# Kernel optimization log

Measured on AMD Instinct MI355X. Metric: run time of the kernel, lower is better.

The kernel has to match this reference:

```python
import jax, jax.numpy as jnp
import numpy as np

RADIUS, HEAD, SLOT, DIM = 16.0, 8, 112, 512

def _l2norm(x, axis):
    n = jnp.linalg.norm(x, axis=axis, keepdims=True)
    return x / jnp.maximum(n, 1e-12)

def _layernorm(x, g, b, eps=1e-5):
    mu = jnp.mean(x, axis=-1, keepdims=True)
    var = jnp.mean((x - mu) ** 2, axis=-1, keepdims=True)
    return (x - mu) / jnp.sqrt(var + eps) * g + b

def setup_inputs() -> dict:
    key = jax.random.key(0)
    ks = jax.random.split(key, 12)
    B, S = 32, 512
    return {
        "query": jax.random.normal(ks[0], (B, S, DIM), jnp.float32),
        "value": jax.random.normal(ks[1], (B, S, DIM), jnp.float32),
        "key_mem": jax.random.normal(ks[2], (HEAD * SLOT, DIM // HEAD), jnp.float32) * 0.5,
        "value_mem": jax.random.normal(ks[3], (SLOT, DIM), jnp.float32) * 0.5,
        "Wq": jax.random.normal(ks[4], (DIM, DIM), jnp.float32) * 0.02,
        "bq": jnp.zeros((DIM,), jnp.float32),
        "Wv": jax.random.normal(ks[5], (DIM, DIM), jnp.float32) * 0.02,
        "bv": jnp.zeros((DIM,), jnp.float32),
        "Wl": jax.random.normal(ks[6], (DIM, DIM * HEAD), jnp.float32) * 0.02,
        "bl": jnp.zeros((DIM,), jnp.float32),
        "g1": jnp.ones((DIM,), jnp.float32), "b1": jnp.zeros((DIM,), jnp.float32),
        "g2": jnp.ones((DIM,), jnp.float32), "b2": jnp.zeros((DIM,), jnp.float32),
        "g3": jnp.ones((DIM,), jnp.float32), "b3": jnp.zeros((DIM,), jnp.float32),
    }

def reference(query, value, key_mem, value_mem, Wq, bq, Wv, bv, Wl, bl,
              g1, b1, g2, b2, g3, b3):
    B, S, C = query.shape
    mq = query.reshape(B * S, C)                                   # (BS, 512)
    # --- key addressing (read path) ---
    key_norm = _l2norm(key_mem.reshape(HEAD, SLOT, -1), axis=2)    # (h, s, 64)
    eq = _l2norm((mq @ Wq.T + bq).reshape(B * S, HEAD, -1), axis=2)
    key_sim = jnp.einsum('bhd,hsd->bhs', eq, key_norm)             # (BS, h, s)
    key_add = jax.nn.softmax(RADIUS * key_sim, axis=2)
    m_head = jnp.einsum('bhs,sd->bhd', key_add,
                        jax.lax.stop_gradient(value_mem))          # (BS, h, 512)
    vir = _layernorm(m_head.reshape(B * S, HEAD * DIM) @ Wl.T + bl, g2, b2)
    te_fusion = _layernorm(query + vir.reshape(B, S, DIM), g1, b1)  # dropout = eval identity
    # --- value addressing (write/train path) ---
    mv = value.reshape(B * S, DIM)
    ev = jax.lax.stop_gradient(mv) @ Wv.T + bv
    value_norm = _l2norm(value_mem, axis=1)                        # (s, 512)
    value_sim = _l2norm(ev, axis=1) @ value_norm.T                 # (BS, s)
    value_add = jax.nn.softmax(RADIUS * value_sim, axis=1)
    aud = value_add @ value_mem                                    # (BS, 512)
    contrastive = 0.5 * jnp.abs(jnp.eye(SLOT, dtype=value_norm.dtype)
                                - value_norm @ value_norm.T).sum()[None]
    mvd = jax.lax.stop_gradient(mv)
    cos = (aud * mvd).sum(1) / jnp.maximum(
        jnp.linalg.norm(aud, axis=1) * jnp.linalg.norm(mvd, axis=1), 1e-8)
    recon = jnp.abs(1.0 - cos).reshape(B, S).sum(1)                # (B,)
    aud = _layernorm(aud, g3, b3)
    tr_fusion = _layernorm(query + aud.reshape(B, S, DIM), g1, b1)
    return (te_fusion, tr_fusion, recon, contrastive)
```

## Files before the change

### kernel.cpp

```cpp
#include <hip/hip_runtime.h>
#include <math.h>

#define DIMC   512
#define HEADS  8
#define SLOTS  112
#define HD     64
#define NROWS  16384
#define RADIUSF 16.0f

typedef short short8 __attribute__((ext_vector_type(8)));
typedef unsigned short ushort8 __attribute__((ext_vector_type(8)));
typedef float f32x4  __attribute__((ext_vector_type(4)));

__device__ __forceinline__ unsigned short f2bf(float f)
{
    unsigned u = __float_as_uint(f);
    unsigned r = (u + 0x7FFFu + ((u >> 16) & 1u)) >> 16;
    return (unsigned short)r;
}
__device__ __forceinline__ float bf2f(unsigned short h)
{
    return __uint_as_float((unsigned)h << 16);
}

#define DPP_ADD(x, ctrl, rmask)                                               \
    (x) += __int_as_float(__builtin_amdgcn_update_dpp(                        \
               0, __float_as_int(x), (ctrl), (rmask), 0xf, true))
#define DPP_MAX(x, ctrl, rmask)                                               \
    (x) = fmaxf((x), __int_as_float(__builtin_amdgcn_update_dpp(              \
               __float_as_int(x), __float_as_int(x), (ctrl), (rmask), 0xf,    \
               false)))

__device__ __forceinline__ float wsum64(float x)
{
    DPP_ADD(x, 0x111, 0xf);
    DPP_ADD(x, 0x112, 0xf);
    DPP_ADD(x, 0x114, 0xf);
    DPP_ADD(x, 0x118, 0xf);
    DPP_ADD(x, 0x142, 0xa);
    DPP_ADD(x, 0x143, 0xc);
    return __int_as_float(__builtin_amdgcn_readlane(__float_as_int(x), 63));
}

__device__ __forceinline__ float wmax64(float x)
{
    DPP_MAX(x, 0x111, 0xf);
    DPP_MAX(x, 0x112, 0xf);
    DPP_MAX(x, 0x114, 0xf);
    DPP_MAX(x, 0x118, 0xf);
    DPP_MAX(x, 0x142, 0xa);
    DPP_MAX(x, 0x143, 0xc);
    return __int_as_float(__builtin_amdgcn_readlane(__float_as_int(x), 63));
}

__device__ __forceinline__ void wsum64_4(float& a, float& b, float& c, float& d)
{
    DPP_ADD(a, 0x111, 0xf); DPP_ADD(b, 0x111, 0xf); DPP_ADD(c, 0x111, 0xf); DPP_ADD(d, 0x111, 0xf);
    DPP_ADD(a, 0x112, 0xf); DPP_ADD(b, 0x112, 0xf); DPP_ADD(c, 0x112, 0xf); DPP_ADD(d, 0x112, 0xf);
    DPP_ADD(a, 0x114, 0xf); DPP_ADD(b, 0x114, 0xf); DPP_ADD(c, 0x114, 0xf); DPP_ADD(d, 0x114, 0xf);
    DPP_ADD(a, 0x118, 0xf); DPP_ADD(b, 0x118, 0xf); DPP_ADD(c, 0x118, 0xf); DPP_ADD(d, 0x118, 0xf);
    DPP_ADD(a, 0x142, 0xa); DPP_ADD(b, 0x142, 0xa); DPP_ADD(c, 0x142, 0xa); DPP_ADD(d, 0x142, 0xa);
    DPP_ADD(a, 0x143, 0xc); DPP_ADD(b, 0x143, 0xc); DPP_ADD(c, 0x143, 0xc); DPP_ADD(d, 0x143, 0xc);
    a = __int_as_float(__builtin_amdgcn_readlane(__float_as_int(a), 63));
    b = __int_as_float(__builtin_amdgcn_readlane(__float_as_int(b), 63));
    c = __int_as_float(__builtin_amdgcn_readlane(__float_as_int(c), 63));
    d = __int_as_float(__builtin_amdgcn_readlane(__float_as_int(d), 63));
}

__device__ __forceinline__ float gsum32(float x)
{
    DPP_ADD(x, 0x111, 0xf);
    DPP_ADD(x, 0x112, 0xf);
    DPP_ADD(x, 0x114, 0xf);
    DPP_ADD(x, 0x118, 0xf);
    DPP_ADD(x, 0x142, 0xa);
    return __shfl(x, 31, 32);
}

__device__ __forceinline__ float gmax32(float x)
{
    DPP_MAX(x, 0x111, 0xf);
    DPP_MAX(x, 0x112, 0xf);
    DPP_MAX(x, 0x114, 0xf);
    DPP_MAX(x, 0x118, 0xf);
    DPP_MAX(x, 0x142, 0xa);
    return __shfl(x, 31, 32);
}

__global__ __launch_bounds__(256)
void gemm_bf16(const short* __restrict__ A, int lda,
               const short* __restrict__ B, int ldb,
               float* __restrict__ C, unsigned short* __restrict__ Cb,
               int ldc, int K, const float* __restrict__ bias, int Nvalid,
               int aZ, int bZ, int cZ)
{
    __shared__ short As[128 * 32];
    __shared__ short Bs[128 * 32];
    A += (size_t)blockIdx.z * aZ;
    B += (size_t)blockIdx.z * bZ;
    const size_t czoff = (size_t)blockIdx.z * cZ;
    const int tid  = threadIdx.x;
    const int wave = tid >> 6;
    const int lane = tid & 63;
    const int m0 = blockIdx.y * 128;
    const int n0 = blockIdx.x * 128;
    const int wm = (wave >> 1) * 64;
    const int wn = (wave & 1) * 64;

    const int srow = tid >> 2;
    const int schk = (tid & 3) * 8;

    const int fr = lane & 15;
    const int fq = (lane >> 4) * 8;

    f32x4 acc[4][4] = {};

    const short* Ag = A + (size_t)(m0 + srow) * lda + schk;
    const short* Bg = B + (size_t)(n0 + srow) * ldb + schk;

    for (int k0 = 0; k0 < K; k0 += 32) {
        *(short8*)&As[srow * 32 + schk]        = *(const short8*)(Ag);
        *(short8*)&As[(srow + 64) * 32 + schk] = *(const short8*)(Ag + (size_t)64 * lda);
        *(short8*)&Bs[srow * 32 + schk]        = *(const short8*)(Bg);
        *(short8*)&Bs[(srow + 64) * 32 + schk] = *(const short8*)(Bg + (size_t)64 * ldb);
        Ag += 32; Bg += 32;
        __syncthreads();
        short8 af[4], bf[4];
        #pragma unroll
        for (int i = 0; i < 4; ++i)
            af[i] = *(const short8*)&As[(wm + i * 16 + fr) * 32 + fq];
        #pragma unroll
        for (int j = 0; j < 4; ++j)
            bf[j] = *(const short8*)&Bs[(wn + j * 16 + fr) * 32 + fq];
        #pragma unroll
        for (int i = 0; i < 4; ++i)
            #pragma unroll
            for (int j = 0; j < 4; ++j)
                acc[i][j] = __builtin_amdgcn_mfma_f32_16x16x32_bf16(
                    af[i], bf[j], acc[i][j], 0, 0, 0);
        __syncthreads();
    }

    const int cr = (lane >> 4) * 4;
    const int cc = lane & 15;
    #pragma unroll
    for (int i = 0; i < 4; ++i) {
        const int grow = m0 + wm + i * 16 + cr;
        #pragma unroll
        for (int j = 0; j < 4; ++j) {
            const int gcol = n0 + wn + j * 16 + cc;
            if (gcol < Nvalid) {
                const float bb = bias ? bias[gcol] : 0.f;
                const size_t base = czoff + (size_t)grow * ldc + gcol;
                #pragma unroll
                for (int r = 0; r < 4; ++r) {
                    const float val = acc[i][j][r] + bb;
                    if (C)  C[base + (size_t)r * ldc]  = val;
                    if (Cb) Cb[base + (size_t)r * ldc] = f2bf(val);
                }
            }
        }
    }
}

__device__ __forceinline__ float block_sum_256(float v, float* red)
{
    #pragma unroll
    for (int off = 32; off; off >>= 1) v += __shfl_down(v, off, 64);
    const int lane = threadIdx.x & 63, wid = threadIdx.x >> 6;
    __syncthreads();
    if (lane == 0) red[wid] = v;
    __syncthreads();
    return red[0] + red[1] + red[2] + red[3];
}

__global__ void zero_small(float* p, int n)
{
    int i = blockIdx.x * blockDim.x + threadIdx.x;
    if (i < n) p[i] = 0.f;
}

__global__ void f32_to_bf16(const float* __restrict__ src,
                            unsigned short* __restrict__ dst, int n)
{
    int i = (blockIdx.x * blockDim.x + threadIdx.x) * 4;
    if (i >= n) return;
    float4 v = *(const float4*)(src + i);
    ushort4 o;
    o.x = f2bf(v.x); o.y = f2bf(v.y); o.z = f2bf(v.z); o.w = f2bf(v.w);
    *(ushort4*)(dst + i) = o;
}

__global__ void prep_key_norm(const float* __restrict__ km,
                              unsigned short* __restrict__ knb)
{
    const int row = blockIdx.x;
    const int h = row >> 7, s = row & 127;
    const int lane = threadIdx.x;
    const float v = (s < SLOTS) ? km[(size_t)(h * SLOTS + s) * HD + lane] : 0.f;
    const float ssum = wsum64(v * v);
    const float inv = 1.f / fmaxf(sqrtf(ssum), 1e-12f);
    knb[(size_t)row * HD + lane] = f2bf(v * inv);
}

__global__ void prep_value_norm(const float* __restrict__ vm,
                                float* __restrict__ vn,
                                unsigned short* __restrict__ vnb,
                                unsigned short* __restrict__ vmTb)
{
    const int row = blockIdx.x;
    const int tid = threadIdx.x;
    __shared__ float red[4];
    const float v0 = vm[(size_t)row * DIMC + tid];
    const float v1 = vm[(size_t)row * DIMC + 256 + tid];
    const float tot = block_sum_256(v0 * v0 + v1 * v1, red);
    const float inv = 1.f / fmaxf(sqrtf(tot), 1e-12f);
    vn[(size_t)row * DIMC + tid]        = v0 * inv;
    vn[(size_t)row * DIMC + 256 + tid]  = v1 * inv;
    vnb[(size_t)row * DIMC + tid]       = f2bf(v0 * inv);
    vnb[(size_t)row * DIMC + 256 + tid] = f2bf(v1 * inv);
    vmTb[(size_t)tid * 128 + row]         = f2bf(v0);
    vmTb[(size_t)(256 + tid) * 128 + row] = f2bf(v1);
}

__global__ void contrastive_kernel(const float* __restrict__ vn, float* __restrict__ outc)
{
    __shared__ float vni[DIMC];
    __shared__ float red[2];
    const int i = blockIdx.x, tid = threadIdx.x;
    for (int d = tid; d < DIMC; d += 128) vni[d] = vn[(size_t)i * DIMC + d];
    __syncthreads();
    float t = 0.f;
    if (tid < SLOTS) {
        const float* r = vn + (size_t)tid * DIMC;
        float dot = 0.f;
        for (int d = 0; d < DIMC; ++d) dot += vni[d] * r[d];
        const float delta = (tid == i) ? 1.f : 0.f;
        t = fabsf(delta - dot);
    }
    #pragma unroll
    for (int off = 32; off; off >>= 1) t += __shfl_down(t, off, 64);
    if ((tid & 63) == 0) red[tid >> 6] = t;
    __syncthreads();
    if (tid == 0) atomicAdd(outc, 0.5f * (red[0] + red[1]));
}

__global__ __launch_bounds__(256)
void eq_head_norms(const unsigned short* __restrict__ eq, float* __restrict__ hinv)
{
    const int wid  = threadIdx.x >> 6;
    const int lane = threadIdx.x & 63;
    const int r = blockIdx.x * 4 + wid;
    const ushort8 u = *(const ushort8*)(eq + (size_t)r * DIMC + lane * 8);
    float s = 0.f;
    #pragma unroll
    for (int i = 0; i < 8; ++i) {
        const float f = bf2f(u[i]);
        s += f * f;
    }
    DPP_ADD(s, 0x111, 0xf);
    DPP_ADD(s, 0x112, 0xf);
    DPP_ADD(s, 0x114, 0xf);
    if ((lane & 7) == 7)
        hinv[(size_t)r * HEADS + (lane >> 3)] = 1.f / fmaxf(sqrtf(s), 1e-12f);
}

__global__ __launch_bounds__(256)
void row_rnorm(const unsigned short* __restrict__ x, float* __restrict__ rinv)
{
    const int wave = threadIdx.x >> 6, lane = threadIdx.x & 63;
    const int r = blockIdx.x * 4 + wave;
    const ushort8 u = *(const ushort8*)(x + (size_t)r * DIMC + lane * 8);
    float s = 0.f;
    #pragma unroll
    for (int i = 0; i < 8; ++i) {
        const float f = bf2f(u[i]);
        s += f * f;
    }
    s = wsum64(s);
    if (lane == 0) rinv[r] = 1.f / fmaxf(sqrtf(s), 1e-12f);
}

__global__ __launch_bounds__(256)
void key_softmax(const float* __restrict__ sim, unsigned short* __restrict__ kadd,
                 const float* __restrict__ hinv)
{
    const int r = blockIdx.x, tid = threadIdx.x;
    const int g = tid >> 5, li = tid & 31;
    const float scale = RADIUSF * hinv[(size_t)r * HEADS + g];
    const float* row = sim + (size_t)r * (HEADS * SLOTS) + g * SLOTS;
    unsigned short* orow = kadd + (size_t)r * (2 * HEADS * SLOTS) + g * SLOTS;

    float v[4];
    #pragma unroll
    for (int u = 0; u < 4; ++u) {
        const int s = li + u * 32;
        v[u] = (s < SLOTS) ? row[s] * scale : -1e30f;
    }
    __syncthreads();
    float mx = gmax32(fmaxf(fmaxf(v[0], v[1]), fmaxf(v[2], v[3])));
    float e[4]; float sum = 0.f;
    #pragma unroll
    for (int u = 0; u < 4; ++u) {
        const int s = li + u * 32;
        e[u] = (s < SLOTS) ? __expf(v[u] - mx) : 0.f;
        sum += e[u];
    }
    sum = gsum32(sum);
    const float invs = 1.f / sum;
    #pragma unroll
    for (int u = 0; u < 4; ++u) {
        const int s = li + u * 32;
        if (s < SLOTS) orow[s] = f2bf(e[u] * invs);
    }
}

__global__ __launch_bounds__(256, 4)
void vir_te_w(const float* __restrict__ vir_pre, const float* __restrict__ query,
              const float* __restrict__ g1, const float* __restrict__ b1,
              const float* __restrict__ g2, const float* __restrict__ b2,
              float* __restrict__ out_te)
{
    const int wave = threadIdx.x >> 6, lane = threadIdx.x & 63;
    const int r0 = blockIdx.x * 8 + wave * 2;
    const int c0 = lane * 8;

    float x[2][8], q[2][8];
    #pragma unroll
    for (int p = 0; p < 2; ++p) {
        const size_t base = (size_t)(r0 + p) * DIMC + c0;
        *(f32x4*)&x[p][0] = *(const f32x4*)(vir_pre + base);
        *(f32x4*)&x[p][4] = *(const f32x4*)(vir_pre + base + 4);
        *(f32x4*)&q[p][0] = *(const f32x4*)(query + base);
        *(f32x4*)&q[p][4] = *(const f32x4*)(query + base + 4);
    }
    float gg2[8], bb2[8], gg1[8], bb1[8];
    *(f32x4*)&gg2[0] = *(const f32x4*)(g2 + c0);
    *(f32x4*)&gg2[4] = *(const f32x4*)(g2 + c0 + 4);
    *(f32x4*)&bb2[0] = *(const f32x4*)(b2 + c0);
    *(f32x4*)&bb2[4] = *(const f32x4*)(b2 + c0 + 4);
    *(f32x4*)&gg1[0] = *(const f32x4*)(g1 + c0);
    *(f32x4*)&gg1[4] = *(const f32x4*)(g1 + c0 + 4);
    *(f32x4*)&bb1[0] = *(const f32x4*)(b1 + c0);
    *(f32x4*)&bb1[4] = *(const f32x4*)(b1 + c0 + 4);

    float s1[2] = {0.f, 0.f}, s2[2] = {0.f, 0.f};
    #pragma unroll
    for (int p = 0; p < 2; ++p)
        #pragma unroll
        for (int i = 0; i < 8; ++i) {
            s1[p] += x[p][i];
            s2[p] += x[p][i] * x[p][i];
        }
    wsum64_4(s1[0], s2[0], s1[1], s2[1]);

    float y[2][8];
    float t1[2] = {0.f, 0.f}, t2[2] = {0.f, 0.f};
    #pragma unroll
    for (int p = 0; p < 2; ++p) {
        const float mu = s1[p] * (1.f / DIMC);
        const float var = s2[p] * (1.f / DIMC) - mu * mu;
        const float rstd = rsqrtf(var + 1e-5f);
        #pragma unroll
        for (int i = 0; i < 8; ++i) {
            const float v = (x[p][i] - mu) * rstd * gg2[i] + bb2[i];
            y[p][i] = q[p][i] + v;
            t1[p] += y[p][i];
            t2[p] += y[p][i] * y[p][i];
        }
    }
    wsum64_4(t1[0], t2[0], t1[1], t2[1]);

    #pragma unroll
    for (int p = 0; p < 2; ++p) {
        const float mu = t1[p] * (1.f / DIMC);
        const float var = t2[p] * (1.f / DIMC) - mu * mu;
        const float rstd = rsqrtf(var + 1e-5f);
        float o[8];
        #pragma unroll
        for (int i = 0; i < 8; ++i)
            o[i] = (y[p][i] - mu) * rstd * gg1[i] + bb1[i];
        const size_t base = (size_t)(r0 + p) * DIMC + c0;
        *(float4*)(out_te + base)     = make_float4(o[0], o[1], o[2], o[3]);
        *(float4*)(out_te + base + 4) = make_float4(o[4], o[5], o[6], o[7]);
    }
}

__global__ __launch_bounds__(256)
void value_softmax_w(const float* __restrict__ vs, unsigned short* __restrict__ vsb,
                     const float* __restrict__ rinv)
{
    const int wave = threadIdx.x >> 6, lane = threadIdx.x & 63;
    const int r = blockIdx.x * 4 + wave;
    const float scale = RADIUSF * rinv[r];
    const float* row = vs + (size_t)r * SLOTS;
    const float v0 = row[lane] * scale;
    const float v1 = (lane < 48) ? row[64 + lane] * scale : -1e30f;
    const float m = wmax64(fmaxf(v0, v1));
    const float e0 = __expf(v0 - m);
    const float e1 = (lane < 48) ? __expf(v1 - m) : 0.f;
    const float s = wsum64(e0 + e1);
    const float inv = 1.f / s;
    unsigned short* ob = vsb + (size_t)r * 128;
    ob[lane] = f2bf(e0 * inv);
    ob[64 + lane] = (lane < 48) ? f2bf(e1 * inv) : (unsigned short)0;
}

__global__ __launch_bounds__(256, 4)
void aud_epilogue_w(const float* __restrict__ aud, const float* __restrict__ value,
                    const float* __restrict__ query,
                    const float* __restrict__ g1, const float* __restrict__ b1,
                    const float* __restrict__ g3, const float* __restrict__ b3,
                    float* __restrict__ out_tr, float* __restrict__ recon)
{
    __shared__ float red[4];
    const int wave = threadIdx.x >> 6, lane = threadIdx.x & 63;
    const int r0 = blockIdx.x * 8 + wave * 2;
    const int c0 = lane * 8;

    float a[2][8], v[2][8], q[2][8];
    #pragma unroll
    for (int p = 0; p < 2; ++p) {
        const size_t base = (size_t)(r0 + p) * DIMC + c0;
        *(f32x4*)&a[p][0] = *(const f32x4*)(aud + base);
        *(f32x4*)&a[p][4] = *(const f32x4*)(aud + base + 4);
        *(f32x4*)&v[p][0] = *(const f32x4*)(value + base);
        *(f32x4*)&v[p][4] = *(const f32x4*)(value + base + 4);
        *(f32x4*)&q[p][0] = *(const f32x4*)(query + base);
        *(f32x4*)&q[p][4] = *(const f32x4*)(query + base + 4);
    }
    float gg3[8], bb3[8], gg1[8], bb1[8];
    *(f32x4*)&gg3[0] = *(const f32x4*)(g3 + c0);
    *(f32x4*)&gg3[4] = *(const f32x4*)(g3 + c0 + 4);
    *(f32x4*)&bb3[0] = *(const f32x4*)(b3 + c0);
    *(f32x4*)&bb3[4] = *(const f32x4*)(b3 + c0 + 4);
    *(f32x4*)&gg1[0] = *(const f32x4*)(g1 + c0);
    *(f32x4*)&gg1[4] = *(const f32x4*)(g1 + c0 + 4);
    *(f32x4*)&bb1[0] = *(const f32x4*)(b1 + c0);
    *(f32x4*)&bb1[4] = *(const f32x4*)(b1 + c0 + 4);

    float dot[2] = {0.f, 0.f}, na[2] = {0.f, 0.f};
    float nv[2] = {0.f, 0.f}, s1[2] = {0.f, 0.f};
    #pragma unroll
    for (int p = 0; p < 2; ++p)
        #pragma unroll
        for (int i = 0; i < 8; ++i) {
            dot[p] += a[p][i] * v[p][i];
            na[p]  += a[p][i] * a[p][i];
            nv[p]  += v[p][i] * v[p][i];
            s1[p]  += a[p][i];
        }
    wsum64_4(dot[0], na[0], nv[0], s1[0]);
    wsum64_4(dot[1], na[1], nv[1], s1[1]);

    float rloc = 0.f;
    #pragma unroll
    for (int p = 0; p < 2; ++p) {
        const float cosv = dot[p] / fmaxf(sqrtf(na[p]) * sqrtf(nv[p]), 1e-8f);
        rloc += fabsf(1.f - cosv);
    }
    if (lane == 0) red[wave] = rloc;

    float y[2][8];
    float t1[2] = {0.f, 0.f}, t2[2] = {0.f, 0.f};
    #pragma unroll
    for (int p = 0; p < 2; ++p) {
        const float mu = s1[p] * (1.f / DIMC);
        const float var = na[p] * (1.f / DIMC) - mu * mu;
        const float rstd = rsqrtf(var + 1e-5f);
        #pragma unroll
        for (int i = 0; i < 8; ++i) {
            const float w = (a[p][i] - mu) * rstd * gg3[i] + bb3[i];
            y[p][i] = q[p][i] + w;
            t1[p] += y[p][i];
            t2[p] += y[p][i] * y[p][i];
        }
    }
    wsum64_4(t1[0], t2[0], t1[1], t2[1]);

    #pragma unroll
    for (int p = 0; p < 2; ++p) {
        const float mu = t1[p] * (1.f / DIMC);
        const float var = t2[p] * (1.f / DIMC) - mu * mu;
        const float rstd = rsqrtf(var + 1e-5f);
        float o[8];
        #pragma unroll
        for (int i = 0; i < 8; ++i)
            o[i] = (y[p][i] - mu) * rstd * gg1[i] + bb1[i];
        const size_t base = (size_t)(r0 + p) * DIMC + c0;
        *(float4*)(out_tr + base)     = make_float4(o[0], o[1], o[2], o[3]);
        *(float4*)(out_tr + base + 4) = make_float4(o[4], o[5], o[6], o[7]);
    }

    __syncthreads();
    if (threadIdx.x == 0)
        atomicAdd(&recon[r0 >> 9], red[0] + red[1] + red[2] + red[3]);
}

extern "C" void kernel_launch(void* const* d_in, const int* in_sizes, int n_in,
                              void* d_out, int out_size, void* d_ws, size_t ws_size,
                              hipStream_t stream)
{
    const float* query = (const float*)d_in[0];
    const float* value = (const float*)d_in[1];
    const float* keym  = (const float*)d_in[2];
    const float* vmem  = (const float*)d_in[3];
    const float* Wq    = (const float*)d_in[4];
    const float* bq    = (const float*)d_in[5];
    const float* Wv    = (const float*)d_in[6];
    const float* bv    = (const float*)d_in[7];
    const float* Wl    = (const float*)d_in[8];
    const float* bl    = (const float*)d_in[9];
    const float* g1    = (const float*)d_in[10];
    const float* b1    = (const float*)d_in[11];
    const float* g2    = (const float*)d_in[12];
    const float* b2    = (const float*)d_in[13];
    const float* g3    = (const float*)d_in[14];
    const float* b3    = (const float*)d_in[15];

    float* out    = (float*)d_out;
    float* out_te = out;
    float* out_tr = out + 8388608;
    float* out_rc = out + 16777216;

    float* ws = (float*)d_ws;
    unsigned short* w_knb  = (unsigned short*)(ws + 0);
    unsigned short* w_vmTb = (unsigned short*)(ws + 32768);
    unsigned short* w_vnb  = (unsigned short*)(ws + 65536);
    float*          w_vn   = ws + 98304;
    unsigned short* w_w2tbf= (unsigned short*)(ws + 155648);
    float*          w_hinv = ws + 385024;
    unsigned short* w_vmbf = (unsigned short*)(ws + 516096);
    unsigned short* w_wlbf = (unsigned short*)(ws + 548864);
    float*          w_big1 = ws + 1597440;
    unsigned short* w_xbf  = (unsigned short*)(ws + 9986048);
    float*          w_sims = ws + 14180352;
    unsigned short* w_kadd = (unsigned short*)(ws + 14180352);
    float*          w_vs   = ws + 14180352;
    unsigned short* w_vsb  = (unsigned short*)(ws + 16015360);
    unsigned short* w_qbf  = (unsigned short*)(ws + 28860416);
    unsigned short* w_wqbf = (unsigned short*)(ws + 33054720);
    float*          w_rinv = ws + 33185792;

    zero_small<<<1, 64, 0, stream>>>(out_rc, 33);
    zero_small<<<256, 256, 0, stream>>>(ws + 32768, 65536);
    zero_small<<<128, 256, 0, stream>>>(ws + 516096, 32768);

    prep_key_norm<<<1024, 64, 0, stream>>>(keym, w_knb);
    prep_value_norm<<<112, 256, 0, stream>>>(vmem, w_vn, w_vnb, w_vmTb);
    contrastive_kernel<<<112, 128, 0, stream>>>(w_vn, out_rc + 32);
    f32_to_bf16<<<2048, 256, 0, stream>>>(Wl, w_wlbf, DIMC * DIMC * HEADS);
    f32_to_bf16<<<56, 256, 0, stream>>>(vmem, w_vmbf, SLOTS * DIMC);
    gemm_bf16<<<dim3(1, 4, 8), 256, 0, stream>>>(
        (const short*)w_wlbf, HEADS * DIMC, (const short*)w_vmbf, DIMC,
        nullptr, w_w2tbf, HEADS * SLOTS, DIMC, nullptr, SLOTS,
        DIMC, 0, SLOTS);

    f32_to_bf16<<<8192, 256, 0, stream>>>(query, w_qbf, NROWS * DIMC);
    f32_to_bf16<<<256, 256, 0, stream>>>(Wq, w_wqbf, DIMC * DIMC);
    gemm_bf16<<<dim3(4, 128), 256, 0, stream>>>(
        (const short*)w_qbf, DIMC, (const short*)w_wqbf, DIMC,
        nullptr, w_xbf, DIMC, DIMC, bq, DIMC, 0, 0, 0);
    eq_head_norms<<<NROWS / 4, 256, 0, stream>>>(w_xbf, w_hinv);
    gemm_bf16<<<dim3(1, 128, 8), 256, 0, stream>>>(
        (const short*)w_xbf, DIMC, (const short*)w_knb, HD,
        w_sims, nullptr, HEADS * SLOTS, HD, nullptr, SLOTS,
        HD, 128 * HD, SLOTS);
    key_softmax<<<NROWS, 256, 0, stream>>>(w_sims, w_kadd, w_hinv);
    gemm_bf16<<<dim3(4, 128), 256, 0, stream>>>(
        (const short*)w_kadd, 2 * HEADS * SLOTS, (const short*)w_w2tbf, HEADS * SLOTS,
        w_big1, nullptr, DIMC, HEADS * SLOTS, bl, DIMC, 0, 0, 0);
    vir_te_w<<<NROWS / 8, 256, 0, stream>>>(w_big1, query, g1, b1, g2, b2, out_te);

    f32_to_bf16<<<8192, 256, 0, stream>>>(value, w_qbf, NROWS * DIMC);
    f32_to_bf16<<<256, 256, 0, stream>>>(Wv, w_wqbf, DIMC * DIMC);
    gemm_bf16<<<dim3(4, 128), 256, 0, stream>>>(
        (const short*)w_qbf, DIMC, (const short*)w_wqbf, DIMC,
        nullptr, w_xbf, DIMC, DIMC, bv, DIMC, 0, 0, 0);
    row_rnorm<<<NROWS / 4, 256, 0, stream>>>(w_xbf, w_rinv);
    gemm_bf16<<<dim3(1, 128), 256, 0, stream>>>(
        (const short*)w_xbf, DIMC, (const short*)w_vnb, DIMC,
        w_vs, nullptr, SLOTS, DIMC, nullptr, SLOTS, 0, 0, 0);
    value_softmax_w<<<NROWS / 4, 256, 0, stream>>>(w_vs, w_vsb, w_rinv);
    gemm_bf16<<<dim3(4, 128), 256, 0, stream>>>(
        (const short*)w_vsb, 128, (const short*)w_vmTb, 128,
        w_big1, nullptr, DIMC, 128, nullptr, DIMC, 0, 0, 0);
    aud_epilogue_w<<<NROWS / 8, 256, 0, stream>>>(
        w_big1, value, query, g1, b1, g3, b3, out_tr, out_rc);
}
```

Before: 402.4 us.

## Fuse similarity GEMMs with softmax and load GEMM tiles via direct global-to-LDS

Adds a gemm_softmax kernel that computes the key/value similarity tiles, stages them in shared memory, and applies the scaled softmax there before writing bf16 probabilities. This removes the fp32 similarity round-trip through global memory and the separate softmax launches. The key-address output is also compacted from a padded layout to its natural width, which shrinks the next GEMM's operand. GEMM tile loads now use global_load_lds to skip the register hop. The risks are the large P tile in LDS, which lowers occupancy, and the scalar per-row softmax loops.

```diff
diff --git a/kernel.cpp b/kernel.cpp
--- a/kernel.cpp
+++ b/kernel.cpp
@@ -23,13 +23,17 @@
     return __uint_as_float((unsigned)h << 16);
 }
 
+__device__ __forceinline__ void gl16(const void* g, void* lds_wave_base)
+{
+    __builtin_amdgcn_global_load_lds(
+        (const __attribute__((address_space(1))) unsigned int*)g,
+        (__attribute__((address_space(3))) unsigned int*)lds_wave_base,
+        16, 0, 0);
+}
+
 #define DPP_ADD(x, ctrl, rmask)                                               \
     (x) += __int_as_float(__builtin_amdgcn_update_dpp(                        \
                0, __float_as_int(x), (ctrl), (rmask), 0xf, true))
-#define DPP_MAX(x, ctrl, rmask)                                               \
-    (x) = fmaxf((x), __int_as_float(__builtin_amdgcn_update_dpp(              \
-               __float_as_int(x), __float_as_int(x), (ctrl), (rmask), 0xf,    \
-               false)))
 
 __device__ __forceinline__ float wsum64(float x)
 {
@@ -39,17 +43,6 @@
     DPP_ADD(x, 0x118, 0xf);
     DPP_ADD(x, 0x142, 0xa);
     DPP_ADD(x, 0x143, 0xc);
-    return __int_as_float(__builtin_amdgcn_readlane(__float_as_int(x), 63));
-}
-
-__device__ __forceinline__ float wmax64(float x)
-{
-    DPP_MAX(x, 0x111, 0xf);
-    DPP_MAX(x, 0x112, 0xf);
-    DPP_MAX(x, 0x114, 0xf);
-    DPP_MAX(x, 0x118, 0xf);
-    DPP_MAX(x, 0x142, 0xa);
-    DPP_MAX(x, 0x143, 0xc);
     return __int_as_float(__builtin_amdgcn_readlane(__float_as_int(x), 63));
 }
 
@@ -65,26 +58,6 @@
     b = __int_as_float(__builtin_amdgcn_readlane(__float_as_int(b), 63));
     c = __int_as_float(__builtin_amdgcn_readlane(__float_as_int(c), 63));
     d = __int_as_float(__builtin_amdgcn_readlane(__float_as_int(d), 63));
-}
-
-__device__ __forceinline__ float gsum32(float x)
-{
-    DPP_ADD(x, 0x111, 0xf);
-    DPP_ADD(x, 0x112, 0xf);
-    DPP_ADD(x, 0x114, 0xf);
-    DPP_ADD(x, 0x118, 0xf);
-    DPP_ADD(x, 0x142, 0xa);
-    return __shfl(x, 31, 32);
-}
-
-__device__ __forceinline__ float gmax32(float x)
-{
-    DPP_MAX(x, 0x111, 0xf);
-    DPP_MAX(x, 0x112, 0xf);
-    DPP_MAX(x, 0x114, 0xf);
-    DPP_MAX(x, 0x118, 0xf);
-    DPP_MAX(x, 0x142, 0xa);
-    return __shfl(x, 31, 32);
 }
 
 __global__ __launch_bounds__(256)
@@ -118,11 +91,16 @@
     const short* Ag = A + (size_t)(m0 + srow) * lda + schk;
     const short* Bg = B + (size_t)(n0 + srow) * ldb + schk;
 
+    short* asL = As + wave * 512;
+    short* asU = As + 2048 + wave * 512;
+    short* bsL = Bs + wave * 512;
+    short* bsU = Bs + 2048 + wave * 512;
+
     for (int k0 = 0; k0 < K; k0 += 32) {
-        *(short8*)&As[srow * 32 + schk]        = *(const short8*)(Ag);
-        *(short8*)&As[(srow + 64) * 32 + schk] = *(const short8*)(Ag + (size_t)64 * lda);
-        *(short8*)&Bs[srow * 32 + schk]        = *(const short8*)(Bg);
-        *(short8*)&Bs[(srow + 64) * 32 + schk] = *(const short8*)(Bg + (size_t)64 * ldb);
+        gl16(Ag, asL);
+        gl16(Ag + (size_t)64 * lda, asU);
+        gl16(Bg, bsL);
+        gl16(Bg + (size_t)64 * ldb, bsU);
         Ag += 32; Bg += 32;
         __syncthreads();
         short8 af[4], bf[4];
@@ -163,6 +141,101 @@
     }
 }
 
+__global__ __launch_bounds__(256)
+void gemm_softmax(const short* __restrict__ A, int lda, int aZ,
+                  const short* __restrict__ B, int ldb, int bZ,
+                  int K,
+                  const float* __restrict__ sc, int scStride,
+                  unsigned short* __restrict__ Ob, int ldo, int oPerZ, int padN)
+{
+    __shared__ short As[128 * 32];
+    __shared__ short Bs[128 * 32];
+    __shared__ float P[128][113];
+    A += (size_t)blockIdx.z * aZ;
+    B += (size_t)blockIdx.z * bZ;
+    const int tid  = threadIdx.x;
+    const int wave = tid >> 6;
+    const int lane = tid & 63;
+    const int m0 = blockIdx.y * 128;
+    const int wm = (wave >> 1) * 64;
+    const int wn = (wave & 1) * 64;
+    const int srow = tid >> 2;
+    const int schk = (tid & 3) * 8;
+    const int fr = lane & 15;
+    const int fq = (lane >> 4) * 8;
+
+    f32x4 acc[4][4] = {};
+
+    const short* Ag = A + (size_t)(m0 + srow) * lda + schk;
+    const short* Bg = B + (size_t)srow * ldb + schk;
+
+    short* asL = As + wave * 512;
+    short* asU = As + 2048 + wave * 512;
+    short* bsL = Bs + wave * 512;
+    short* bsU = Bs + 2048 + wave * 512;
+
+    for (int k0 = 0; k0 < K; k0 += 32) {
+        gl16(Ag, asL);
+        gl16(Ag + (size_t)64 * lda, asU);
+        gl16(Bg, bsL);
+        gl16(Bg + (size_t)64 * ldb, bsU);
+        Ag += 32; Bg += 32;
+        __syncthreads();
+        short8 af[4], bf[4];
+        #pragma unroll
+        for (int i = 0; i < 4; ++i)
+            af[i] = *(const short8*)&As[(wm + i * 16 + fr) * 32 + fq];
+        #pragma unroll
+        for (int j = 0; j < 4; ++j)
+            bf[j] = *(const short8*)&Bs[(wn + j * 16 + fr) * 32 + fq];
+        #pragma unroll
+        for (int i = 0; i < 4; ++i)
+            #pragma unroll
+            for (int j = 0; j < 4; ++j)
+                acc[i][j] = __builtin_amdgcn_mfma_f32_16x16x32_bf16(
+                    af[i], bf[j], acc[i][j], 0, 0, 0);
+        __syncthreads();
+    }
+
+    const int cr = (lane >> 4) * 4;
+    const int cc = lane & 15;
+    #pragma unroll
+    for (int i = 0; i < 4; ++i) {
+        const int prow = wm + i * 16 + cr;
+        #pragma unroll
+        for (int j = 0; j < 4; ++j) {
+            const int pcol = wn + j * 16 + cc;
+            if (pcol < SLOTS) {
+                #pragma unroll
+                for (int r = 0; r < 4; ++r)
+                    P[prow + r][pcol] = acc[i][j][r];
+            }
+        }
+    }
+    __syncthreads();
+
+    const int rowt = tid >> 1;
+    const int half = tid & 1;
+    const int k0 = half * 56;
+    const int rr = m0 + rowt;
+    const float s = RADIUSF * sc[(size_t)rr * scStride + blockIdx.z];
+    float mx = -1e30f;
+    for (int k = k0; k < k0 + 56; ++k) mx = fmaxf(mx, P[rowt][k]);
+    mx = fmaxf(mx, __shfl_xor(mx, 1, 64));
+    float sum = 0.f;
+    for (int k = k0; k < k0 + 56; ++k) {
+        const float e = __expf(s * (P[rowt][k] - mx));
+        P[rowt][k] = e;
+        sum += e;
+    }
+    sum += __shfl_xor(sum, 1, 64);
+    const float inv = 1.f / sum;
+    unsigned short* orow = Ob + (size_t)rr * ldo + (size_t)blockIdx.z * oPerZ;
+    for (int k = k0; k < k0 + 56; ++k) orow[k] = f2bf(P[rowt][k] * inv);
+    if (half == 1)
+        for (int k = SLOTS; k < padN; ++k) orow[k] = 0;
+}
+
 __device__ __forceinline__ float block_sum_256(float v, float* red)
 {
     #pragma unroll
@@ -281,40 +354,6 @@
     if (lane == 0) rinv[r] = 1.f / fmaxf(sqrtf(s), 1e-12f);
 }
 
-__global__ __launch_bounds__(256)
-void key_softmax(const float* __restrict__ sim, unsigned short* __restrict__ kadd,
-                 const float* __restrict__ hinv)
-{
-    const int r = blockIdx.x, tid = threadIdx.x;
-    const int g = tid >> 5, li = tid & 31;
-    const float scale = RADIUSF * hinv[(size_t)r * HEADS + g];
-    const float* row = sim + (size_t)r * (HEADS * SLOTS) + g * SLOTS;
-    unsigned short* orow = kadd + (size_t)r * (2 * HEADS * SLOTS) + g * SLOTS;
-
-    float v[4];
-    #pragma unroll
-    for (int u = 0; u < 4; ++u) {
-        const int s = li + u * 32;
-        v[u] = (s < SLOTS) ? row[s] * scale : -1e30f;
-    }
-    __syncthreads();
-    float mx = gmax32(fmaxf(fmaxf(v[0], v[1]), fmaxf(v[2], v[3])));
-    float e[4]; float sum = 0.f;
-    #pragma unroll
-    for (int u = 0; u < 4; ++u) {
-        const int s = li + u * 32;
-        e[u] = (s < SLOTS) ? __expf(v[u] - mx) : 0.f;
-        sum += e[u];
-    }
-    sum = gsum32(sum);
-    const float invs = 1.f / sum;
-    #pragma unroll
-    for (int u = 0; u < 4; ++u) {
-        const int s = li + u * 32;
-        if (s < SLOTS) orow[s] = f2bf(e[u] * invs);
-    }
-}
-
 __global__ __launch_bounds__(256, 4)
 void vir_te_w(const float* __restrict__ vir_pre, const float* __restrict__ query,
               const float* __restrict__ g1, const float* __restrict__ b1,
@@ -384,26 +423,6 @@
         *(float4*)(out_te + base)     = make_float4(o[0], o[1], o[2], o[3]);
         *(float4*)(out_te + base + 4) = make_float4(o[4], o[5], o[6], o[7]);
     }
-}
-
-__global__ __launch_bounds__(256)
-void value_softmax_w(const float* __restrict__ vs, unsigned short* __restrict__ vsb,
-                     const float* __restrict__ rinv)
-{
-    const int wave = threadIdx.x >> 6, lane = threadIdx.x & 63;
-    const int r = blockIdx.x * 4 + wave;
-    const float scale = RADIUSF * rinv[r];
-    const float* row = vs + (size_t)r * SLOTS;
-    const float v0 = row[lane] * scale;
-    const float v1 = (lane < 48) ? row[64 + lane] * scale : -1e30f;
-    const float m = wmax64(fmaxf(v0, v1));
-    const float e0 = __expf(v0 - m);
-    const float e1 = (lane < 48) ? __expf(v1 - m) : 0.f;
-    const float s = wsum64(e0 + e1);
-    const float inv = 1.f / s;
-    unsigned short* ob = vsb + (size_t)r * 128;
-    ob[lane] = f2bf(e0 * inv);
-    ob[64 + lane] = (lane < 48) ? f2bf(e1 * inv) : (unsigned short)0;
 }
 
 __global__ __launch_bounds__(256, 4)
@@ -534,13 +553,11 @@
     unsigned short* w_wlbf = (unsigned short*)(ws + 548864);
     float*          w_big1 = ws + 1597440;
     unsigned short* w_xbf  = (unsigned short*)(ws + 9986048);
-    float*          w_sims = ws + 14180352;
-    unsigned short* w_kadd = (unsigned short*)(ws + 14180352);
-    float*          w_vs   = ws + 14180352;
-    unsigned short* w_vsb  = (unsigned short*)(ws + 16015360);
-    unsigned short* w_qbf  = (unsigned short*)(ws + 28860416);
-    unsigned short* w_wqbf = (unsigned short*)(ws + 33054720);
-    float*          w_rinv = ws + 33185792;
+    unsigned short* w_kaddc= (unsigned short*)(ws + 14180352);
+    unsigned short* w_vsb  = (unsigned short*)(ws + 21520384);
+    unsigned short* w_qbf  = (unsigned short*)(ws + 22568960);
+    unsigned short* w_wqbf = (unsigned short*)(ws + 26763264);
+    float*          w_rinv = ws + 26894336;
 
     zero_small<<<1, 64, 0, stream>>>(out_rc, 33);
     zero_small<<<256, 256, 0, stream>>>(ws + 32768, 65536);
@@ -562,13 +579,11 @@
         (const short*)w_qbf, DIMC, (const short*)w_wqbf, DIMC,
         nullptr, w_xbf, DIMC, DIMC, bq, DIMC, 0, 0, 0);
     eq_head_norms<<<NROWS / 4, 256, 0, stream>>>(w_xbf, w_hinv);
-    gemm_bf16<<<dim3(1, 128, 8), 256, 0, stream>>>(
-        (const short*)w_xbf, DIMC, (const short*)w_knb, HD,
-        w_sims, nullptr, HEADS * SLOTS, HD, nullptr, SLOTS,
-        HD, 128 * HD, SLOTS);
-    key_softmax<<<NROWS, 256, 0, stream>>>(w_sims, w_kadd, w_hinv);
+    gemm_softmax<<<dim3(1, 128, 8), 256, 0, stream>>>(
+        (const short*)w_xbf, DIMC, HD, (const short*)w_knb, HD, 128 * HD,
+        HD, w_hinv, HEADS, w_kaddc, HEADS * SLOTS, SLOTS, SLOTS);
     gemm_bf16<<<dim3(4, 128), 256, 0, stream>>>(
-        (const short*)w_kadd, 2 * HEADS * SLOTS, (const short*)w_w2tbf, HEADS * SLOTS,
+        (const short*)w_kaddc, HEADS * SLOTS, (const short*)w_w2tbf, HEADS * SLOTS,
         w_big1, nullptr, DIMC, HEADS * SLOTS, bl, DIMC, 0, 0, 0);
     vir_te_w<<<NROWS / 8, 256, 0, stream>>>(w_big1, query, g1, b1, g2, b2, out_te);
 
@@ -578,10 +593,9 @@
         (const short*)w_qbf, DIMC, (const short*)w_wqbf, DIMC,
         nullptr, w_xbf, DIMC, DIMC, bv, DIMC, 0, 0, 0);
     row_rnorm<<<NROWS / 4, 256, 0, stream>>>(w_xbf, w_rinv);
-    gemm_bf16<<<dim3(1, 128), 256, 0, stream>>>(
-        (const short*)w_xbf, DIMC, (const short*)w_vnb, DIMC,
-        w_vs, nullptr, SLOTS, DIMC, nullptr, SLOTS, 0, 0, 0);
-    value_softmax_w<<<NROWS / 4, 256, 0, stream>>>(w_vs, w_vsb, w_rinv);
+    gemm_softmax<<<dim3(1, 128, 1), 256, 0, stream>>>(
+        (const short*)w_xbf, DIMC, 0, (const short*)w_vnb, DIMC, 0,
+        DIMC, w_rinv, 1, w_vsb, 128, 0, 128);
     gemm_bf16<<<dim3(4, 128), 256, 0, stream>>>(
         (const short*)w_vsb, 128, (const short*)w_vmTb, 128,
         w_big1, nullptr, DIMC, 128, nullptr, DIMC, 0, 0, 0);
```

Result: faster. 388.2 us (-3.5%).
